# Optimization experiments

Hardware: AMD Instinct MI355X
Metric: run time of the kernel (lower is better)

## Reference

```python
import jax, jax.numpy as jnp
import numpy as np

NUM_ITEMS = 100000
HIDDEN = 128
NNZ = 1600000


def setup_inputs() -> dict:
    key = jax.random.key(0)
    k1, k2, k3, k4, k5, k6 = jax.random.split(key, 6)
    item_embedding_table = jax.random.normal(k1, (NUM_ITEMS, HIDDEN), dtype=jnp.float32)
    adj_rows = jnp.sort(jax.random.randint(k2, (NNZ,), 0, NUM_ITEMS, dtype=jnp.int32))
    adj_cols = jax.random.randint(k3, (NNZ,), 0, NUM_ITEMS, dtype=jnp.int32)
    adj_vals = jax.random.uniform(k4, (NNZ,), dtype=jnp.float32)
    # nn.Linear default init (uniform in +-1/sqrt(fan_in)) approximated by scaled normal
    W_weight = jax.random.normal(k5, (HIDDEN, HIDDEN), dtype=jnp.float32) / np.sqrt(HIDDEN)
    W_bias = jax.random.normal(k6, (HIDDEN,), dtype=jnp.float32) * 0.01
    return {
        "item_embedding_table": item_embedding_table,
        "adj_rows": adj_rows,
        "adj_cols": adj_cols,
        "adj_vals": adj_vals,
        "W_weight": W_weight,
        "W_bias": W_bias,
    }


def reference(item_embedding_table, adj_rows, adj_cols, adj_vals, W_weight, W_bias):
    # support = W(x): x @ W^T + b   (nn.Linear convention: weight [out, in])
    support = jnp.einsum("nd,hd->nh", item_embedding_table, W_weight) + W_bias  # [N, H]
    # output = sparse_coo(adj) @ support, via gather + segment-sum scatter
    msgs = adj_vals[:, None] * support[adj_cols]  # [nnz, H]
    output = jax.ops.segment_sum(msgs, adj_rows, num_segments=NUM_ITEMS)  # [N, H]
    return output
```

## Files before the change

kernel.cpp:

```cpp
#include <hip/hip_runtime.h>

#define N_ITEMS 100000
#define HID 128
#define NNZ_T 1600000
#define EPW 128
#define WPB 4
#define PF 8

typedef unsigned short ushort_t;
typedef unsigned int uint_t;
typedef short bf16x8 __attribute__((ext_vector_type(8)));
typedef float f32x4 __attribute__((ext_vector_type(4)));

static __device__ __forceinline__ ushort_t f32_to_bf16(float f) {
    uint_t u = __float_as_uint(f);
    uint_t r = (u + 0x7FFFu + ((u >> 16) & 1u)) >> 16;
    return (ushort_t)r;
}

__global__ void prep_w(const float* __restrict__ W, ushort_t* __restrict__ Wb) {
    int i = blockIdx.x * blockDim.x + threadIdx.x;
    Wb[i] = f32_to_bf16(W[i]);
}

__global__ __launch_bounds__(256) void gemm_mfma(
    const float* __restrict__ X, const ushort_t* __restrict__ Wb,
    const float* __restrict__ bias, ushort_t* __restrict__ S) {
    const int lane = threadIdx.x & 63;
    const int wave = threadIdx.x >> 6;
    const int m = lane & 15;
    const int q = lane >> 4;
    const int row0 = blockIdx.x * 64 + wave * 16;

    int arow = row0 + m;
    if (arow >= N_ITEMS) arow = N_ITEMS - 1;

    f32x4 acc[8] = {};

#pragma unroll
    for (int kb = 0; kb < 4; ++kb) {
        const int k0 = kb * 32 + q * 8;
        float4 a0 = *(const float4*)&X[(size_t)arow * HID + k0];
        float4 a1 = *(const float4*)&X[(size_t)arow * HID + k0 + 4];
        bf16x8 af;
        af[0] = (short)f32_to_bf16(a0.x); af[1] = (short)f32_to_bf16(a0.y);
        af[2] = (short)f32_to_bf16(a0.z); af[3] = (short)f32_to_bf16(a0.w);
        af[4] = (short)f32_to_bf16(a1.x); af[5] = (short)f32_to_bf16(a1.y);
        af[6] = (short)f32_to_bf16(a1.z); af[7] = (short)f32_to_bf16(a1.w);
#pragma unroll
        for (int nt = 0; nt < 8; ++nt) {
            bf16x8 bfr = *(const bf16x8*)&Wb[(size_t)(nt * 16 + m) * HID + k0];
            acc[nt] = __builtin_amdgcn_mfma_f32_16x16x32_bf16(af, bfr, acc[nt], 0, 0, 0);
        }
    }

#pragma unroll
    for (int nt = 0; nt < 8; ++nt) {
        const int col = nt * 16 + m;
        const float bv = bias[col];
#pragma unroll
        for (int r = 0; r < 4; ++r) {
            const int row = row0 + q * 4 + r;
            if (row < N_ITEMS)
                S[(size_t)row * HID + col] = f32_to_bf16(acc[nt][r] + bv);
        }
    }
}

__global__ __launch_bounds__(WPB * 64) void spmm(
    const int* __restrict__ rows, const int* __restrict__ cols,
    const float* __restrict__ vals, const ushort_t* __restrict__ S,
    float* __restrict__ out) {
    __shared__ int   s_row[WPB * EPW];
    __shared__ uint2 s_cv[WPB * EPW];

    const int tid = threadIdx.x;
    const int e0 = blockIdx.x * (WPB * EPW);
    for (int i = tid; i < WPB * EPW; i += WPB * 64) {
        s_row[i] = rows[e0 + i];
        s_cv[i] = make_uint2((uint_t)cols[e0 + i], __float_as_uint(vals[e0 + i]));
    }
    __syncthreads();

    const int wave = tid >> 6;
    const int lane = tid & 63;
    const int base0 = wave * EPW;

    float2 acc = make_float2(0.f, 0.f);
    int cur = s_row[base0];
    bool first = true;

    for (int g = 0; g < EPW; g += PF) {
        uint_t u[PF];
#pragma unroll
        for (int i = 0; i < PF; ++i) {
            uint_t c = s_cv[base0 + g + i].x;
            u[i] = *(const uint_t*)&S[(size_t)c * HID + 2 * lane];
        }
#pragma unroll
        for (int i = 0; i < PF; ++i) {
            const int e = base0 + g + i;
            const int r = s_row[e];
            if (r != cur) {
                float* p = &out[(size_t)cur * HID + 2 * lane];
                if (first) { atomicAdd(p, acc.x); atomicAdd(p + 1, acc.y); }
                else       { *(float2*)p = acc; }
                first = false;
                acc = make_float2(0.f, 0.f);
                cur = r;
            }
            const float v = __uint_as_float(s_cv[e].y);
            const float f0 = __uint_as_float(u[i] << 16);
            const float f1 = __uint_as_float(u[i] & 0xFFFF0000u);
            acc.x = fmaf(v, f0, acc.x);
            acc.y = fmaf(v, f1, acc.y);
        }
    }
    float* p = &out[(size_t)cur * HID + 2 * lane];
    atomicAdd(p, acc.x); atomicAdd(p + 1, acc.y);
}

extern "C" void kernel_launch(void* const* d_in, const int* in_sizes, int n_in,
                              void* d_out, int out_size, void* d_ws, size_t ws_size,
                              hipStream_t stream) {
    const float* X    = (const float*)d_in[0];
    const int*   rows = (const int*)  d_in[1];
    const int*   cols = (const int*)  d_in[2];
    const float* vals = (const float*)d_in[3];
    const float* W    = (const float*)d_in[4];
    const float* bias = (const float*)d_in[5];
    float* out = (float*)d_out;

    ushort_t* Wb = (ushort_t*)d_ws;
    ushort_t* S  = Wb + HID * HID;

    hipMemsetAsync(d_out, 0, (size_t)out_size * sizeof(float), stream);
    prep_w<<<(HID * HID) / 256, 256, 0, stream>>>(W, Wb);
    gemm_mfma<<<(N_ITEMS + 63) / 64, 256, 0, stream>>>(X, Wb, bias, S);
    spmm<<<NNZ_T / (WPB * EPW), WPB * 64, 0, stream>>>(rows, cols, vals, S, out);
}
```

Measured before the change: 219.0 us.

## Double-buffer SpMM edge batches in registers instead of staging through LDS

The SpMM kernel no longer stages rows/cols/vals into shared memory with a block-wide barrier. Each wave now loads its own edge metadata directly with uniform (scalar-friendly) loads, and uses two register buffers so the gather for the next batch of 8 edges is in flight while the current batch is accumulated. This aims to hide gather latency and drop the LDS traffic and syncthreads, at the cost of higher register pressure.

```diff
diff --git a/kernel.cpp b/kernel.cpp
--- a/kernel.cpp
+++ b/kernel.cpp
@@ -4,8 +4,8 @@
 #define HID 128
 #define NNZ_T 1600000
 #define EPW 128
-#define WPB 4
-#define PF 8
+#define BATCH 8
+#define NBATCH (EPW / BATCH)
 
 typedef unsigned short ushort_t;
 typedef unsigned int uint_t;
@@ -67,54 +67,58 @@
     }
 }
 
-__global__ __launch_bounds__(WPB * 64) void spmm(
+__global__ __launch_bounds__(256) void spmm(
     const int* __restrict__ rows, const int* __restrict__ cols,
     const float* __restrict__ vals, const ushort_t* __restrict__ S,
     float* __restrict__ out) {
-    __shared__ int   s_row[WPB * EPW];
-    __shared__ uint2 s_cv[WPB * EPW];
+    const int lane = threadIdx.x & 63;
+    const int wv = __builtin_amdgcn_readfirstlane(threadIdx.x >> 6);
+    const int e0 = (blockIdx.x * 4 + wv) * EPW;
 
-    const int tid = threadIdx.x;
-    const int e0 = blockIdx.x * (WPB * EPW);
-    for (int i = tid; i < WPB * EPW; i += WPB * 64) {
-        s_row[i] = rows[e0 + i];
-        s_cv[i] = make_uint2((uint_t)cols[e0 + i], __float_as_uint(vals[e0 + i]));
-    }
-    __syncthreads();
-
-    const int wave = tid >> 6;
-    const int lane = tid & 63;
-    const int base0 = wave * EPW;
+    int    rA[BATCH], cA[BATCH]; float vA[BATCH]; uint_t uA[BATCH];
+    int    rB[BATCH], cB[BATCH]; float vB[BATCH]; uint_t uB[BATCH];
 
     float2 acc = make_float2(0.f, 0.f);
-    int cur = s_row[base0];
+    int cur;
     bool first = true;
 
-    for (int g = 0; g < EPW; g += PF) {
-        uint_t u[PF];
+    auto fetch = [&](int g, int* r, int* c, float* v, uint_t* u) {
+        const int eb = e0 + g * BATCH;
 #pragma unroll
-        for (int i = 0; i < PF; ++i) {
-            uint_t c = s_cv[base0 + g + i].x;
-            u[i] = *(const uint_t*)&S[(size_t)c * HID + 2 * lane];
+        for (int j = 0; j < BATCH; ++j) {
+            r[j] = rows[eb + j];
+            c[j] = cols[eb + j];
+            v[j] = vals[eb + j];
         }
 #pragma unroll
-        for (int i = 0; i < PF; ++i) {
-            const int e = base0 + g + i;
-            const int r = s_row[e];
-            if (r != cur) {
+        for (int j = 0; j < BATCH; ++j)
+            u[j] = *(const uint_t*)&S[(size_t)c[j] * HID + 2 * lane];
+    };
+    auto consume = [&](const int* r, const float* v, const uint_t* u) {
+#pragma unroll
+        for (int j = 0; j < BATCH; ++j) {
+            if (r[j] != cur) {
                 float* p = &out[(size_t)cur * HID + 2 * lane];
                 if (first) { atomicAdd(p, acc.x); atomicAdd(p + 1, acc.y); }
                 else       { *(float2*)p = acc; }
                 first = false;
                 acc = make_float2(0.f, 0.f);
-                cur = r;
+                cur = r[j];
             }
-            const float v = __uint_as_float(s_cv[e].y);
-            const float f0 = __uint_as_float(u[i] << 16);
-            const float f1 = __uint_as_float(u[i] & 0xFFFF0000u);
-            acc.x = fmaf(v, f0, acc.x);
-            acc.y = fmaf(v, f1, acc.y);
+            const float f0 = __uint_as_float(u[j] << 16);
+            const float f1 = __uint_as_float(u[j] & 0xFFFF0000u);
+            acc.x = fmaf(v[j], f0, acc.x);
+            acc.y = fmaf(v[j], f1, acc.y);
         }
+    };
+
+    fetch(0, rA, cA, vA, uA);
+    cur = rA[0];
+    for (int g = 0; g < NBATCH; g += 2) {
+        if (g + 1 < NBATCH) fetch(g + 1, rB, cB, vB, uB);
+        consume(rA, vA, uA);
+        if (g + 2 < NBATCH) fetch(g + 2, rA, cA, vA, uA);
+        consume(rB, vB, uB);
     }
     float* p = &out[(size_t)cur * HID + 2 * lane];
     atomicAdd(p, acc.x); atomicAdd(p + 1, acc.y);
@@ -137,5 +141,5 @@
     hipMemsetAsync(d_out, 0, (size_t)out_size * sizeof(float), stream);
     prep_w<<<(HID * HID) / 256, 256, 0, stream>>>(W, Wb);
     gemm_mfma<<<(N_ITEMS + 63) / 64, 256, 0, stream>>>(X, Wb, bias, S);
-    spmm<<<NNZ_T / (WPB * EPW), WPB * 64, 0, stream>>>(rows, cols, vals, S, out);
+    spmm<<<NNZ_T / (4 * EPW), 256, 0, stream>>>(rows, cols, vals, S, out);
 }
```

Result: slower. 238.9 us (+9.1%).

## Convert COO SpMM to CSR row-per-wave with binary-searched row pointers

Applied to the files above, without the earlier changes.

Builds a CSR row_ptr array by binary search over the sorted row indices. The SpMM then runs one wave per output row and writes each row directly, with no atomics and no separate memset of the output. This removes the atomic adds at segment boundaries and the output memset, but adds a rowptr kernel and uneven work per wave because row lengths vary. Column and value loads are now per-lane scalar loads from global memory instead of being staged through LDS.

```diff
diff --git a/kernel.cpp b/kernel.cpp
--- a/kernel.cpp
+++ b/kernel.cpp
@@ -3,9 +3,6 @@
 #define N_ITEMS 100000
 #define HID 128
 #define NNZ_T 1600000
-#define EPW 128
-#define WPB 4
-#define PF 8
 
 typedef unsigned short ushort_t;
 typedef unsigned int uint_t;
@@ -21,6 +18,17 @@
 __global__ void prep_w(const float* __restrict__ W, ushort_t* __restrict__ Wb) {
     int i = blockIdx.x * blockDim.x + threadIdx.x;
     Wb[i] = f32_to_bf16(W[i]);
+}
+
+__global__ void build_rowptr(const int* __restrict__ rows, int* __restrict__ row_ptr) {
+    int r = blockIdx.x * blockDim.x + threadIdx.x;
+    if (r > N_ITEMS) return;
+    int lo = 0, hi = NNZ_T;
+    while (lo < hi) {
+        int mid = (lo + hi) >> 1;
+        if (rows[mid] < r) lo = mid + 1; else hi = mid;
+    }
+    row_ptr[r] = lo;
 }
 
 __global__ __launch_bounds__(256) void gemm_mfma(
@@ -67,57 +75,41 @@
     }
 }
 
-__global__ __launch_bounds__(WPB * 64) void spmm(
-    const int* __restrict__ rows, const int* __restrict__ cols,
-    const float* __restrict__ vals, const ushort_t* __restrict__ S,
+__global__ __launch_bounds__(256) void spmm_csr(
+    const int* __restrict__ cols, const float* __restrict__ vals,
+    const int* __restrict__ row_ptr, const ushort_t* __restrict__ S,
     float* __restrict__ out) {
-    __shared__ int   s_row[WPB * EPW];
-    __shared__ uint2 s_cv[WPB * EPW];
+    const int lane = threadIdx.x & 63;
+    const int row = blockIdx.x * 4 + (int)__builtin_amdgcn_readfirstlane(threadIdx.x >> 6);
+    if (row >= N_ITEMS) return;
 
-    const int tid = threadIdx.x;
-    const int e0 = blockIdx.x * (WPB * EPW);
-    for (int i = tid; i < WPB * EPW; i += WPB * 64) {
-        s_row[i] = rows[e0 + i];
-        s_cv[i] = make_uint2((uint_t)cols[e0 + i], __float_as_uint(vals[e0 + i]));
-    }
-    __syncthreads();
-
-    const int wave = tid >> 6;
-    const int lane = tid & 63;
-    const int base0 = wave * EPW;
+    const int p0 = row_ptr[row];
+    const int p1 = row_ptr[row + 1];
 
     float2 acc = make_float2(0.f, 0.f);
-    int cur = s_row[base0];
-    bool first = true;
-
-    for (int g = 0; g < EPW; g += PF) {
-        uint_t u[PF];
+    int p = p0;
+    for (; p + 8 <= p1; p += 8) {
+        uint_t u[8]; float v[8];
 #pragma unroll
-        for (int i = 0; i < PF; ++i) {
-            uint_t c = s_cv[base0 + g + i].x;
-            u[i] = *(const uint_t*)&S[(size_t)c * HID + 2 * lane];
+        for (int j = 0; j < 8; ++j) {
+            int c = cols[p + j];
+            v[j] = vals[p + j];
+            u[j] = *(const uint_t*)&S[(size_t)c * HID + 2 * lane];
         }
 #pragma unroll
-        for (int i = 0; i < PF; ++i) {
-            const int e = base0 + g + i;
-            const int r = s_row[e];
-            if (r != cur) {
-                float* p = &out[(size_t)cur * HID + 2 * lane];
-                if (first) { atomicAdd(p, acc.x); atomicAdd(p + 1, acc.y); }
-                else       { *(float2*)p = acc; }
-                first = false;
-                acc = make_float2(0.f, 0.f);
-                cur = r;
-            }
-            const float v = __uint_as_float(s_cv[e].y);
-            const float f0 = __uint_as_float(u[i] << 16);
-            const float f1 = __uint_as_float(u[i] & 0xFFFF0000u);
-            acc.x = fmaf(v, f0, acc.x);
-            acc.y = fmaf(v, f1, acc.y);
+        for (int j = 0; j < 8; ++j) {
+            acc.x = fmaf(v[j], __uint_as_float(u[j] << 16), acc.x);
+            acc.y = fmaf(v[j], __uint_as_float(u[j] & 0xFFFF0000u), acc.y);
         }
     }
-    float* p = &out[(size_t)cur * HID + 2 * lane];
-    atomicAdd(p, acc.x); atomicAdd(p + 1, acc.y);
+    for (; p < p1; ++p) {
+        int c = cols[p];
+        float v = vals[p];
+        uint_t u = *(const uint_t*)&S[(size_t)c * HID + 2 * lane];
+        acc.x = fmaf(v, __uint_as_float(u << 16), acc.x);
+        acc.y = fmaf(v, __uint_as_float(u & 0xFFFF0000u), acc.y);
+    }
+    *(float2*)&out[(size_t)row * HID + 2 * lane] = acc;
 }
 
 extern "C" void kernel_launch(void* const* d_in, const int* in_sizes, int n_in,
@@ -131,11 +123,12 @@
     const float* bias = (const float*)d_in[5];
     float* out = (float*)d_out;
 
-    ushort_t* Wb = (ushort_t*)d_ws;
-    ushort_t* S  = Wb + HID * HID;
+    ushort_t* Wb      = (ushort_t*)d_ws;
+    ushort_t* S       = Wb + HID * HID;
+    int*      row_ptr = (int*)(S + (size_t)N_ITEMS * HID);
 
-    hipMemsetAsync(d_out, 0, (size_t)out_size * sizeof(float), stream);
     prep_w<<<(HID * HID) / 256, 256, 0, stream>>>(W, Wb);
+    build_rowptr<<<(N_ITEMS + 256) / 256, 256, 0, stream>>>(rows, row_ptr);
     gemm_mfma<<<(N_ITEMS + 63) / 64, 256, 0, stream>>>(X, Wb, bias, S);
-    spmm<<<NNZ_T / (WPB * EPW), WPB * 64, 0, stream>>>(rows, cols, vals, S, out);
+    spmm_csr<<<(N_ITEMS + 3) / 4, 256, 0, stream>>>(cols, vals, row_ptr, S, out);
 }
```

After: 222.6 us. No clear change (+1.6%).
